# Performance work log

Measured on AMD Instinct MI355X. Metric: run time of the kernel, lower is better.

## Reference

```python
import jax, jax.numpy as jnp
import numpy as np
import math

N_CELLS = 65536
HIDDEN = 128
IN_DIM = 64
MAX_DEG = 6
BOND_P = 0.5


def _build_graph():
    """2D lattice bond percolation -> padded adjacency [n, MAX_DEG] + signs + mask."""
    rng = np.random.default_rng(0)
    side = int(math.ceil(math.sqrt(N_CELLS)))
    adj = [[] for _ in range(N_CELLS)]
    for i in range(N_CELLS):
        col = i % side
        r = i + 1
        if col + 1 < side and r < N_CELLS and rng.random() < BOND_P:
            adj[i].append(r); adj[r].append(i)
        d = i + side
        if d < N_CELLS and rng.random() < BOND_P:
            adj[i].append(d); adj[d].append(i)
    for i in range(N_CELLS):  # ring fix for isolated nodes
        if not adj[i]:
            r = (i + 1) % N_CELLS
            adj[i].append(r); adj[r].append(i)
    sign_map = {}
    for i in range(N_CELLS):
        for j in adj[i]:
            key = (min(i, j), max(i, j))
            if key not in sign_map:
                sign_map[key] = 1.0 if rng.random() > 0.5 else -1.0
    nbr = np.zeros((N_CELLS, MAX_DEG), np.int32)
    sgn = np.ones((N_CELLS, MAX_DEG), np.float32)
    msk = np.zeros((N_CELLS, MAX_DEG), bool)
    for i in range(N_CELLS):
        for k, j in enumerate(adj[i][:MAX_DEG]):
            nbr[i, k] = j
            msk[i, k] = True
            sgn[i, k] = sign_map[(min(i, j), max(i, j))]
    return nbr, sgn, msk


def setup_inputs() -> dict:
    key = jax.random.key(0)
    ks = jax.random.split(key, 8)
    nbr, sgn, msk = _build_graph()
    n = N_CELLS
    cell_amp = jax.random.uniform(ks[0], (n, HIDDEN)) * 0.5 + 0.5
    cell_phase = jax.random.normal(ks[1], (n, HIDDEN)) * 0.5 \
        + (2.0 * jnp.pi * jnp.arange(n, dtype=jnp.float32) / n)[:, None]
    phase_vel = jax.random.normal(ks[2], (n, HIDDEN)) * 0.05
    return {
        'x': jax.random.normal(ks[3], (1, IN_DIM)),
        'cell_amp': cell_amp.astype(jnp.float32),
        'cell_phase': cell_phase.astype(jnp.float32),
        'phase_vel': phase_vel.astype(jnp.float32),
        'nbr_idx': jnp.asarray(nbr),
        'nbr_sign': jnp.asarray(sgn),
        'nbr_mask': jnp.asarray(msk),
        'W_in': jax.random.normal(ks[4], (HIDDEN, IN_DIM)) * 0.05,
        'b_in': jax.random.normal(ks[5], (HIDDEN,)) * 0.05,
        'W_dec': jax.random.normal(ks[6], (IN_DIM, 2 * HIDDEN)) * 0.05,
        'b_dec': jax.random.normal(ks[7], (IN_DIM,)) * 0.05,
        'step': 1,
    }


def reference(x, cell_amp, cell_phase, phase_vel, nbr_idx, nbr_sign, nbr_mask,
              W_in, b_in, W_dec, b_dec, step):
    n, h = cell_amp.shape
    # complex cell states, then phase-velocity rotation
    states = (cell_amp * jnp.exp(1j * cell_phase)).astype(jnp.complex64)
    states = states * jnp.exp(1j * phase_vel * 0.1)
    ang = jnp.angle(states)                               # [n, h]

    # --- neighbor interference (vectorized gather over padded adjacency) ---
    nbr_states = states[nbr_idx]                          # [n, d, h]
    nbr_ang = ang[nbr_idx]                                # [n, d, h]
    coupling = jnp.cos(ang[:, None, :] - nbr_ang) * nbr_sign[:, :, None]
    contrib = jnp.where(nbr_mask[:, :, None], coupling * nbr_states * 0.1, 0.0)
    interference = contrib.sum(axis=1)                    # [n, h]
    deg = nbr_mask.sum(axis=-1)                           # [n]
    new = 0.7 * states + 0.3 * interference / jnp.maximum(deg, 1)[:, None]
    new = jnp.where((deg > 0)[:, None], new, states)      # 'continue' for isolated nodes

    # --- morphism toward strongest neighbor (argmax over neighbors) ---
    strength = jnp.abs(states).sum(axis=-1)               # [n]
    nstr = jnp.where(nbr_mask, strength[nbr_idx], -jnp.inf)
    best_slot = jnp.argmax(nstr, axis=1)                  # first max, like python max()
    best = jnp.take_along_axis(nbr_idx, best_slot[:, None], axis=1)[:, 0]
    src = states[best]                                    # [n, h]
    morph = jnp.abs(src) * jnp.exp(1j * (jnp.angle(new) - jnp.angle(src)))
    new = jnp.where((deg >= 2)[:, None], new + 0.02 * morph, new)

    # --- global traveling wave ---
    t = step * 0.1
    wave = 0.02 * jnp.sin(t + 2.0 * jnp.pi * jnp.arange(n, dtype=jnp.float32) / n)
    new = new * (1.0 + wave)[:, None]

    # --- input-driven phase perturbation on first 32 cells ---
    sig = x[0] @ W_in.T + b_in                            # [h]
    pp = sig / (jnp.abs(sig).max() + 1e-8) * jnp.pi * 0.1
    idx = jnp.arange(n, dtype=jnp.float32)
    factor = jnp.where(jnp.arange(n) < 32, 0.1 / (1.0 + 0.1 * idx), 0.0)
    new_ang = jnp.angle(new) + pp[None, :] * factor[:, None]
    new = jnp.abs(new) * jnp.exp(1j * new_ang)

    # --- amplitude renormalization per cell ---
    amp = jnp.abs(new)
    amp = amp / (amp.max(axis=-1, keepdims=True) + 1e-8)
    cs = (amp * jnp.exp(1j * jnp.angle(new))).astype(jnp.complex64)

    # --- readout ---
    mean_state = cs.mean(axis=0)                          # [h]
    out_real = jnp.concatenate([mean_state.real, mean_state.imag])[None, :]
    pred = out_real @ W_dec.T + b_dec                     # [1, IN_DIM]
    tension = jnp.var(jnp.abs(cs), ddof=1)                # torch.var (unbiased)
    return pred, tension
```

## Files before the change

kernel.cpp:

```cpp
#include <hip/hip_runtime.h>
#include <hip/hip_fp16.h>
#include <math.h>

#define N_CELLS 65536
#define HIDDEN  128
#define IN_DIM  64
#define MAX_DEG 6

#define WPB    4
#define NPB    32
#define NBLK   (N_CELLS/NPB)
#define CHUNK  4
#define NXCD   8

#define INV2PI 0.15915494309189535f

typedef _Float16 h2f __attribute__((ext_vector_type(2)));

__device__ __forceinline__ void fsincos(float x, float& s, float& c) {
    const float r = x * INV2PI;
    s = __builtin_amdgcn_sinf(r);
    c = __builtin_amdgcn_cosf(r);
}

#define WS_PP    0
#define WS_FLAG  512
#define WS_STR   1024
#define WS_S     (1024 + N_CELLS*4)
#define WS_ADJ   (WS_S + (size_t)N_CELLS*512)
#define WS_P     (WS_ADJ + (size_t)N_CELLS*32)
#define WS_SA    (WS_P + 256*NBLK*4)
#define WS_SA2   (WS_SA + NBLK*4)
#define WS_MEAN  (WS_SA2 + NBLK*4)

__global__ __launch_bounds__(256) void k_pre(
    const float* __restrict__ amp, const float* __restrict__ phase,
    const float* __restrict__ vel,
    const float* __restrict__ x, const float* __restrict__ W_in,
    const float* __restrict__ b_in, const unsigned char* __restrict__ maskb,
    int4* __restrict__ S, float* __restrict__ strength,
    float* __restrict__ pp, int* __restrict__ flag)
{
    const int tid = threadIdx.x;
    const int bx  = blockIdx.x;
    if (bx < N_CELLS/8) {
        const int blkp = (bx & (NXCD-1)) * (N_CELLS/8/NXCD) + (bx >> 3);
        const int node = blkp*8 + (tid >> 5);
        const int hl   = tid & 31;
        const size_t ro = (size_t)node*HIDDEN + 4*hl;
        const float4 a = *(const float4*)(amp   + ro);
        const float4 p = *(const float4*)(phase + ro);
        const float4 v = *(const float4*)(vel   + ro);
        float s0,c0,s1,c1,s2,c2,s3,c3;
        fsincos(fmaf(0.1f, v.x, p.x), s0, c0);
        fsincos(fmaf(0.1f, v.y, p.y), s1, c1);
        fsincos(fmaf(0.1f, v.z, p.z), s2, c2);
        fsincos(fmaf(0.1f, v.w, p.w), s3, c3);
        union { int4 v4; __half2 h[4]; } u;
        u.h[0] = __floats2half2_rn(a.x*c0, a.x*s0);
        u.h[1] = __floats2half2_rn(a.y*c1, a.y*s1);
        u.h[2] = __floats2half2_rn(a.z*c2, a.z*s2);
        u.h[3] = __floats2half2_rn(a.w*c3, a.w*s3);
        S[(size_t)node*32 + hl] = u.v4;
        float st = a.x + a.y + a.z + a.w;
        #pragma unroll
        for (int off = 16; off > 0; off >>= 1) st += __shfl_xor(st, off);
        if (hl == 0) strength[node] = st;
        return;
    }
    __shared__ float sig[HIDDEN];
    __shared__ float red[HIDDEN];
    __shared__ int fl[256];
    if (tid < HIDDEN) {
        float acc = b_in[tid];
        #pragma unroll 8
        for (int d = 0; d < IN_DIM; ++d) acc = fmaf(W_in[tid*IN_DIM + d], x[d], acc);
        sig[tid] = acc;
        red[tid] = fabsf(acc);
    }
    int v = 0;
    #pragma unroll
    for (int r = 0; r < 4; ++r) v |= (int)maskb[(tid + 256*r)*4 + 1];
    fl[tid] = v;
    __syncthreads();
    for (int s = 64; s > 0; s >>= 1) {
        if (tid < s) red[tid] = fmaxf(red[tid], red[tid + s]);
        __syncthreads();
    }
    for (int s = 128; s > 0; s >>= 1) {
        if (tid < s) fl[tid] |= fl[tid + s];
        __syncthreads();
    }
    if (tid < HIDDEN) pp[tid] = sig[tid] / (red[0] + 1e-8f) * 0.314159265358979f;
    if (tid == 0) *flag = (fl[0] != 0) ? 1 : 0;
}

__global__ __launch_bounds__(256) void k_adj(
    const int* __restrict__ nbr_idx, const float* __restrict__ nbr_sign,
    const void* __restrict__ nbr_mask, const int* __restrict__ flagp,
    const float* __restrict__ strength, int4* __restrict__ adj)
{
    __shared__ int   lw[256][MAX_DEG];
    __shared__ float ls[256][MAX_DEG];
    __shared__ int   ldeg[256];
    const int t = threadIdx.x;
    const int bx = blockIdx.x;
    const int blkp = (bx & (NXCD-1)) * (N_CELLS/256/NXCD) + (bx >> 3);
    const int i = blkp*256 + t;
    const int flagv = *flagp;
    const unsigned char* mb = (const unsigned char*)nbr_mask;
    const int*           mi = (const int*)nbr_mask;
    int cnt = 0;
    #pragma unroll
    for (int k = 0; k < MAX_DEG; ++k) {
        const int e = i*MAX_DEG + k;
        const int m = flagv ? (mb[e] != 0) : (mi[e] != 0);
        const int j = nbr_idx[e];
        const float sg = nbr_sign[e];
        if (m) {
            lw[t][cnt] = j | ((sg < 0.0f) ? (1<<24) : 0) | (1<<25);
            ls[t][cnt] = strength[j];
            ++cnt;
        }
    }
    int cb = 0; float bv = ls[t][0];
    #pragma unroll
    for (int k = 1; k < MAX_DEG; ++k)
        if (k < cnt && ls[t][k] > bv) { bv = ls[t][k]; cb = k; }
    if (cb != 0) {
        const int tmp = lw[t][0];
        lw[t][0] = lw[t][cb];
        lw[t][cb] = tmp;
    }
    #pragma unroll
    for (int k = 0; k < MAX_DEG; ++k) if (k >= cnt) lw[t][k] = i;
    ldeg[t] = cnt;
    __syncthreads();
    const int kmax = max(cnt, ldeg[t ^ 1]);
    adj[2*(size_t)i    ] = make_int4(lw[t][0], lw[t][1], lw[t][2], lw[t][3]);
    adj[2*(size_t)i + 1] = make_int4(lw[t][4], lw[t][5], cnt, kmax);
}

__global__ __launch_bounds__(256) void k_mainc(
    const int4* __restrict__ S, const int4* __restrict__ adj,
    const int* __restrict__ step, const float* __restrict__ pp,
    float* __restrict__ P, float* __restrict__ p_sa, float* __restrict__ p_sa2)
{
    __shared__ float4 lredre[WPB][32], lredim[WPB][32];
    __shared__ float  lsa[WPB], lsa2[WPB];

    const int tid   = threadIdx.x;
    const int bx    = blockIdx.x;
    const int blk   = (bx & (NXCD-1)) * (NBLK/NXCD) + (bx >> 3);
    const int node0 = blk * NPB;

    const int wv   = tid >> 6;
    const int lane = tid & 63;
    const int half = lane >> 5;
    const int lh   = lane & 31;
    const float trev = 0.1f * (float)step[0] * INV2PI;
    const float4 ppv = ((const float4*)pp)[lh];

    float accre[4] = {0,0,0,0}, accim[4] = {0,0,0,0};
    float accsa = 0.f, accsa2 = 0.f;

    const int nlbase = wv*(2*CHUNK) + half;
    int4 A0n = adj[2*(size_t)(node0 + nlbase)    ];
    int4 A1n = adj[2*(size_t)(node0 + nlbase) + 1];

    #pragma unroll 1
    for (int c = 0; c < CHUNK; ++c) {
        const int nl = nlbase + 2*c;
        const int i  = node0 + nl;
        const int4 A0 = A0n, A1 = A1n;
        if (c + 1 < CHUNK) {
            A0n = adj[2*(size_t)(i + 2)    ];
            A1n = adj[2*(size_t)(i + 2) + 1];
        }
        const int deg  = A1.z;
        const int kmax = __builtin_amdgcn_readfirstlane(A1.w);
        const int slots[MAX_DEG] = {A0.x, A0.y, A0.z, A0.w, A1.x, A1.y};

        union H { int4 v4; h2f h[4]; int w[4]; };
        H us, nb[MAX_DEG];
        us.v4 = S[(size_t)(unsigned)i*32 + lh];
        #pragma unroll
        for (int k = 0; k < MAX_DEG; ++k)
            if (k < kmax) nb[k].v4 = S[(size_t)(unsigned)(slots[k] & 0xFFFF)*32 + lh];

        float R[4], I[4], inva[4];
        #pragma unroll
        for (int q = 0; q < 4; ++q) {
            R[q] = (float)us.h[q].x;
            I[q] = (float)us.h[q].y;
            inva[q] = __builtin_amdgcn_rsqf(
                __builtin_amdgcn_fdot2(us.h[q], us.h[q], 0.0f, false));
        }

        float ir[4] = {0,0,0,0}, ii[4] = {0,0,0,0};
        #pragma unroll
        for (int k = 0; k < MAX_DEG; ++k) {
            if (k < kmax) {
                const int w = slots[k];
                const float vf = (float)((w >> 25) & 1);
                const float sgnm = (w & (1<<24)) ? -vf : vf;
                #pragma unroll
                for (int q = 0; q < 4; ++q) {
                    const float E   = __builtin_amdgcn_fdot2(us.h[q], nb[k].h[q], 0.0f, false);
                    const float aj2 = __builtin_amdgcn_fdot2(nb[k].h[q], nb[k].h[q], 0.0f, false);
                    const float g = sgnm * E * __builtin_amdgcn_rsqf(aj2);
                    ir[q] = fmaf(g, (float)nb[k].h[q].x, ir[q]);
                    ii[q] = fmaf(g, (float)nb[k].h[q].y, ii[q]);
                }
            }
        }

        const float f = 0.03f * __builtin_amdgcn_rcpf((float)deg);
        float nr[4], ni[4];
        #pragma unroll
        for (int q = 0; q < 4; ++q) {
            const float fq = f * inva[q];
            nr[q] = fmaf(0.7f, R[q], fq*ir[q]);
            ni[q] = fmaf(0.7f, I[q], fq*ii[q]);
        }

        const float g2 = (deg >= 2) ? 0.02f : 0.0f;
        #pragma unroll
        for (int q = 0; q < 4; ++q) {
            const float ex = (float)nb[0].h[q].x, ey = (float)nb[0].h[q].y;
            const float im = g2 * __builtin_amdgcn_rsqf(
                fmaxf(nr[q]*nr[q] + ni[q]*ni[q], 1e-30f));
            const float mr = im*(nr[q]*ex + ni[q]*ey);
            const float mi = im*(ni[q]*ex - nr[q]*ey);
            nr[q] += mr; ni[q] += mi;
        }

        const float wr = fmaf((float)i, 1.52587890625e-5f, trev);
        const float wf = 1.0f + 0.02f * __builtin_amdgcn_sinf(wr);
        #pragma unroll
        for (int q = 0; q < 4; ++q) { nr[q] *= wf; ni[q] *= wf; }

        if (i < 32) {
            const float fac = 0.1f / fmaf(0.1f, (float)i, 1.0f);
            const float pv[4] = {ppv.x, ppv.y, ppv.z, ppv.w};
            #pragma unroll
            for (int q = 0; q < 4; ++q) {
                float sp, cp;
                fsincos(pv[q]*fac, sp, cp);
                const float tr = nr[q]*cp - ni[q]*sp;
                ni[q] = ni[q]*cp + nr[q]*sp;
                nr[q] = tr;
            }
        }

        float m[4];
        #pragma unroll
        for (int q = 0; q < 4; ++q) m[q] = sqrtf(nr[q]*nr[q] + ni[q]*ni[q]);
        float lm = fmaxf(fmaxf(m[0], m[1]), fmaxf(m[2], m[3]));
        #pragma unroll
        for (int off = 16; off > 0; off >>= 1) lm = fmaxf(lm, __shfl_xor(lm, off));
        const float sc = 1.0f / (lm + 1e-8f);
        #pragma unroll
        for (int q = 0; q < 4; ++q) {
            accre[q] += nr[q]*sc;
            accim[q] += ni[q]*sc;
            const float A = m[q]*sc;
            accsa  += A;
            accsa2 += A*A;
        }
    }

    #pragma unroll
    for (int q = 0; q < 4; ++q) {
        accre[q] += __shfl_xor(accre[q], 32);
        accim[q] += __shfl_xor(accim[q], 32);
    }
    #pragma unroll
    for (int off = 32; off > 0; off >>= 1) {
        accsa  += __shfl_xor(accsa,  off);
        accsa2 += __shfl_xor(accsa2, off);
    }
    if (half == 0) {
        lredre[wv][lh] = make_float4(accre[0], accre[1], accre[2], accre[3]);
        lredim[wv][lh] = make_float4(accim[0], accim[1], accim[2], accim[3]);
    }
    if (lane == 0) { lsa[wv] = accsa; lsa2[wv] = accsa2; }
    __syncthreads();
    if (tid < 32) {
        float4 r = lredre[0][tid], im = lredim[0][tid];
        #pragma unroll
        for (int w = 1; w < WPB; ++w) {
            const float4 a = lredre[w][tid], b = lredim[w][tid];
            r.x += a.x; r.y += a.y; r.z += a.z; r.w += a.w;
            im.x += b.x; im.y += b.y; im.z += b.z; im.w += b.w;
        }
        P[(4*tid  )*NBLK + blk]       = r.x;
        P[(4*tid+1)*NBLK + blk]       = r.y;
        P[(4*tid+2)*NBLK + blk]       = r.z;
        P[(4*tid+3)*NBLK + blk]       = r.w;
        P[(128+4*tid  )*NBLK + blk]   = im.x;
        P[(128+4*tid+1)*NBLK + blk]   = im.y;
        P[(128+4*tid+2)*NBLK + blk]   = im.z;
        P[(128+4*tid+3)*NBLK + blk]   = im.w;
    }
    if (tid == 0) {
        p_sa [blk] = lsa[0]  + lsa[1]  + lsa[2]  + lsa[3];
        p_sa2[blk] = lsa2[0] + lsa2[1] + lsa2[2] + lsa2[3];
    }
}

__global__ void k_red(const float* __restrict__ P, float* __restrict__ mean)
{
    __shared__ double red[256];
    const int r = blockIdx.x, tid = threadIdx.x;
    double s = 0.0;
    #pragma unroll
    for (int k = 0; k < NBLK/256; ++k) s += (double)P[(size_t)r*NBLK + tid + 256*k];
    red[tid] = s;
    __syncthreads();
    for (int st = 128; st > 0; st >>= 1) { if (tid < st) red[tid] += red[tid + st]; __syncthreads(); }
    if (tid == 0) mean[r] = (float)(red[0] / (double)N_CELLS);
}

__global__ void k_final(const float* __restrict__ mean_in,
                        const float* __restrict__ p_sa, const float* __restrict__ p_sa2,
                        const float* __restrict__ W_dec, const float* __restrict__ b_dec,
                        float* __restrict__ out)
{
    __shared__ float  mean[2*HIDDEN];
    __shared__ double dred[256];
    __shared__ double tots[2];
    const int tid = threadIdx.x;
    mean[tid] = mean_in[tid];
    double sa = 0.0, sa2 = 0.0;
    #pragma unroll
    for (int k = 0; k < NBLK/256; ++k) {
        sa  += (double)p_sa [tid + 256*k];
        sa2 += (double)p_sa2[tid + 256*k];
    }
    dred[tid] = sa;
    __syncthreads();
    for (int s = 128; s > 0; s >>= 1) { if (tid < s) dred[tid] += dred[tid + s]; __syncthreads(); }
    if (tid == 0) tots[0] = dred[0];
    __syncthreads();
    dred[tid] = sa2;
    __syncthreads();
    for (int s = 128; s > 0; s >>= 1) { if (tid < s) dred[tid] += dred[tid + s]; __syncthreads(); }
    if (tid == 0) tots[1] = dred[0];
    __syncthreads();

    if (tid < IN_DIM) {
        float acc = b_dec[tid];
        #pragma unroll 8
        for (int c = 0; c < 2*HIDDEN; ++c) acc = fmaf(mean[c], W_dec[tid*2*HIDDEN + c], acc);
        out[tid] = acc;
    }
    if (tid == 0) {
        const double M = (double)N_CELLS * (double)HIDDEN;
        const double var = (tots[1] - tots[0]*tots[0]/M) / (M - 1.0);
        out[IN_DIM] = (float)var;
    }
}

extern "C" void kernel_launch(void* const* d_in, const int* in_sizes, int n_in,
                              void* d_out, int out_size, void* d_ws, size_t ws_size,
                              hipStream_t stream)
{
    const float* x       = (const float*)d_in[0];
    const float* amp     = (const float*)d_in[1];
    const float* phase   = (const float*)d_in[2];
    const float* vel     = (const float*)d_in[3];
    const int*   nbr_idx = (const int*)d_in[4];
    const float* nbr_sgn = (const float*)d_in[5];
    const void*  nbr_msk = d_in[6];
    const float* W_in    = (const float*)d_in[7];
    const float* b_in    = (const float*)d_in[8];
    const float* W_dec   = (const float*)d_in[9];
    const float* b_dec   = (const float*)d_in[10];
    const int*   step    = (const int*)d_in[11];

    char* wsb = (char*)d_ws;
    float* pp    = (float*)(wsb + WS_PP);
    int*   flag  = (int*)  (wsb + WS_FLAG);
    float* strg  = (float*)(wsb + WS_STR);
    int4*  S     = (int4*) (wsb + WS_S);
    int4*  adjv  = (int4*) (wsb + WS_ADJ);
    float* P     = (float*)(wsb + WS_P);
    float* p_sa  = (float*)(wsb + WS_SA);
    float* p_sa2 = (float*)(wsb + WS_SA2);
    float* meanb = (float*)(wsb + WS_MEAN);
    float* out   = (float*)d_out;

    k_pre<<<N_CELLS/8 + 1, 256, 0, stream>>>(amp, phase, vel, x, W_in, b_in,
                                             (const unsigned char*)nbr_msk,
                                             S, strg, pp, flag);
    k_adj<<<N_CELLS/256, 256, 0, stream>>>(nbr_idx, nbr_sgn, nbr_msk, flag, strg, adjv);
    k_mainc<<<NBLK, 256, 0, stream>>>(S, adjv, step, pp, P, p_sa, p_sa2);
    k_red<<<256, 256, 0, stream>>>(P, meanb);
    k_final<<<1, 256, 0, stream>>>(meanb, p_sa, p_sa2, W_dec, b_dec, out);
}
```

Baseline: 66.43 us.

## Store unit phasors alongside complex state to drop per-neighbor rsqrt normalization

```diff
diff --git a/kernel.cpp b/kernel.cpp
--- a/kernel.cpp
+++ b/kernel.cpp
@@ -26,8 +26,8 @@
 #define WS_PP    0
 #define WS_FLAG  512
 #define WS_STR   1024
-#define WS_S     (1024 + N_CELLS*4)
-#define WS_ADJ   (WS_S + (size_t)N_CELLS*512)
+#define WS_S2    (1024 + N_CELLS*4)
+#define WS_ADJ   (WS_S2 + (size_t)N_CELLS*1024)
 #define WS_P     (WS_ADJ + (size_t)N_CELLS*32)
 #define WS_SA    (WS_P + 256*NBLK*4)
 #define WS_SA2   (WS_SA + NBLK*4)
@@ -38,7 +38,7 @@
     const float* __restrict__ vel,
     const float* __restrict__ x, const float* __restrict__ W_in,
     const float* __restrict__ b_in, const unsigned char* __restrict__ maskb,
-    int4* __restrict__ S, float* __restrict__ strength,
+    int4* __restrict__ S2, float* __restrict__ strength,
     float* __restrict__ pp, int* __restrict__ flag)
 {
     const int tid = threadIdx.x;
@@ -56,12 +56,18 @@
         fsincos(fmaf(0.1f, v.y, p.y), s1, c1);
         fsincos(fmaf(0.1f, v.z, p.z), s2, c2);
         fsincos(fmaf(0.1f, v.w, p.w), s3, c3);
-        union { int4 v4; __half2 h[4]; } u;
-        u.h[0] = __floats2half2_rn(a.x*c0, a.x*s0);
-        u.h[1] = __floats2half2_rn(a.y*c1, a.y*s1);
-        u.h[2] = __floats2half2_rn(a.z*c2, a.z*s2);
-        u.h[3] = __floats2half2_rn(a.w*c3, a.w*s3);
-        S[(size_t)node*32 + hl] = u.v4;
+        union { int4 v4; __half2 h[4]; } uu, vv;
+        uu.h[0] = __floats2half2_rn(c0, s0);
+        uu.h[1] = __floats2half2_rn(c1, s1);
+        uu.h[2] = __floats2half2_rn(c2, s2);
+        uu.h[3] = __floats2half2_rn(c3, s3);
+        vv.h[0] = __floats2half2_rn(a.x*c0, a.x*s0);
+        vv.h[1] = __floats2half2_rn(a.y*c1, a.y*s1);
+        vv.h[2] = __floats2half2_rn(a.z*c2, a.z*s2);
+        vv.h[3] = __floats2half2_rn(a.w*c3, a.w*s3);
+        const size_t base = ((size_t)node*32 + hl)*2;
+        S2[base]     = uu.v4;
+        S2[base + 1] = vv.v4;
         float st = a.x + a.y + a.z + a.w;
         #pragma unroll
         for (int off = 16; off > 0; off >>= 1) st += __shfl_xor(st, off);
@@ -142,7 +148,7 @@
 }
 
 __global__ __launch_bounds__(256) void k_mainc(
-    const int4* __restrict__ S, const int4* __restrict__ adj,
+    const int4* __restrict__ S2, const int4* __restrict__ adj,
     const int* __restrict__ step, const float* __restrict__ pp,
     float* __restrict__ P, float* __restrict__ p_sa, float* __restrict__ p_sa2)
 {
@@ -181,23 +187,23 @@
         const int kmax = __builtin_amdgcn_readfirstlane(A1.w);
         const int slots[MAX_DEG] = {A0.x, A0.y, A0.z, A0.w, A1.x, A1.y};
 
-        union H { int4 v4; h2f h[4]; int w[4]; };
-        H us, nb[MAX_DEG];
-        us.v4 = S[(size_t)(unsigned)i*32 + lh];
-        #pragma unroll
-        for (int k = 0; k < MAX_DEG; ++k)
-            if (k < kmax) nb[k].v4 = S[(size_t)(unsigned)(slots[k] & 0xFFFF)*32 + lh];
-
-        float R[4], I[4], inva[4];
-        #pragma unroll
-        for (int q = 0; q < 4; ++q) {
-            R[q] = (float)us.h[q].x;
-            I[q] = (float)us.h[q].y;
-            inva[q] = __builtin_amdgcn_rsqf(
-                __builtin_amdgcn_fdot2(us.h[q], us.h[q], 0.0f, false));
-        }
-
-        float ir[4] = {0,0,0,0}, ii[4] = {0,0,0,0};
+        union H { int4 v4; h2f h[4]; };
+        H su, sv, nu[MAX_DEG], nv[MAX_DEG];
+        const size_t sb = ((size_t)(unsigned)i*32 + lh)*2;
+        su.v4 = S2[sb];
+        sv.v4 = S2[sb + 1];
+        #pragma unroll
+        for (int k = 0; k < MAX_DEG; ++k) {
+            if (k < kmax) {
+                const size_t jb = ((size_t)(unsigned)(slots[k] & 0xFFFF)*32 + lh)*2;
+                nu[k].v4 = S2[jb];
+                nv[k].v4 = S2[jb + 1];
+            }
+        }
+
+        h2f acc[4];
+        #pragma unroll
+        for (int q = 0; q < 4; ++q) acc[q] = (h2f){(_Float16)0.f, (_Float16)0.f};
         #pragma unroll
         for (int k = 0; k < MAX_DEG; ++k) {
             if (k < kmax) {
@@ -206,11 +212,10 @@
                 const float sgnm = (w & (1<<24)) ? -vf : vf;
                 #pragma unroll
                 for (int q = 0; q < 4; ++q) {
-                    const float E   = __builtin_amdgcn_fdot2(us.h[q], nb[k].h[q], 0.0f, false);
-                    const float aj2 = __builtin_amdgcn_fdot2(nb[k].h[q], nb[k].h[q], 0.0f, false);
-                    const float g = sgnm * E * __builtin_amdgcn_rsqf(aj2);
-                    ir[q] = fmaf(g, (float)nb[k].h[q].x, ir[q]);
-                    ii[q] = fmaf(g, (float)nb[k].h[q].y, ii[q]);
+                    const float cosD = __builtin_amdgcn_fdot2(su.h[q], nu[k].h[q], 0.0f, false);
+                    const _Float16 t = (_Float16)(cosD * sgnm);
+                    const h2f tv = (h2f){t, t};
+                    acc[q] = tv * nv[k].h[q] + acc[q];
                 }
             }
         }
@@ -219,15 +224,14 @@
         float nr[4], ni[4];
         #pragma unroll
         for (int q = 0; q < 4; ++q) {
-            const float fq = f * inva[q];
-            nr[q] = fmaf(0.7f, R[q], fq*ir[q]);
-            ni[q] = fmaf(0.7f, I[q], fq*ii[q]);
+            nr[q] = fmaf(0.7f, (float)sv.h[q].x, f*(float)acc[q].x);
+            ni[q] = fmaf(0.7f, (float)sv.h[q].y, f*(float)acc[q].y);
         }
 
         const float g2 = (deg >= 2) ? 0.02f : 0.0f;
         #pragma unroll
         for (int q = 0; q < 4; ++q) {
-            const float ex = (float)nb[0].h[q].x, ey = (float)nb[0].h[q].y;
+            const float ex = (float)nv[0].h[q].x, ey = (float)nv[0].h[q].y;
             const float im = g2 * __builtin_amdgcn_rsqf(
                 fmaxf(nr[q]*nr[q] + ni[q]*ni[q], 1e-30f));
             const float mr = im*(nr[q]*ex + ni[q]*ey);
@@ -383,7 +387,7 @@
     float* pp    = (float*)(wsb + WS_PP);
     int*   flag  = (int*)  (wsb + WS_FLAG);
     float* strg  = (float*)(wsb + WS_STR);
-    int4*  S     = (int4*) (wsb + WS_S);
+    int4*  S2    = (int4*) (wsb + WS_S2);
     int4*  adjv  = (int4*) (wsb + WS_ADJ);
     float* P     = (float*)(wsb + WS_P);
     float* p_sa  = (float*)(wsb + WS_SA);
@@ -393,9 +397,9 @@
 
     k_pre<<<N_CELLS/8 + 1, 256, 0, stream>>>(amp, phase, vel, x, W_in, b_in,
                                              (const unsigned char*)nbr_msk,
-                                             S, strg, pp, flag);
+                                             S2, strg, pp, flag);
     k_adj<<<N_CELLS/256, 256, 0, stream>>>(nbr_idx, nbr_sgn, nbr_msk, flag, strg, adjv);
-    k_mainc<<<NBLK, 256, 0, stream>>>(S, adjv, step, pp, P, p_sa, p_sa2);
+    k_mainc<<<NBLK, 256, 0, stream>>>(S2, adjv, step, pp, P, p_sa, p_sa2);
     k_red<<<256, 256, 0, stream>>>(P, meanb);
     k_final<<<1, 256, 0, stream>>>(meanb, p_sa, p_sa2, W_dec, b_dec, out);
 }
```

Result: slower. 70.69 us (+6.4%).
